# Optimization experiments

Hardware: AMD Instinct MI355X
Metric: run time of the kernel (lower is better)

The kernel has to match this reference:

```python
import jax, jax.numpy as jnp
import numpy as np


def _laplacian_with_self_loop(adj):
    # matrix = adj + I; D^{-1/2} (sym-normalized) as in the torch code
    n = adj.shape[0]
    m = adj + jnp.eye(n, dtype=adj.dtype)
    row_sum = m.sum(axis=1)
    d_inv_sqrt = row_sum ** -0.5
    d_inv_sqrt = jnp.where(jnp.isinf(d_inv_sqrt), 0.0, d_inv_sqrt)
    # (m @ diag(d)).T @ diag(d) == (m * d[None,:]).T * d[None,:]
    return (m * d_inv_sqrt[None, :]).T * d_inv_sqrt[None, :]


MAX_DIFFUSION_STEP = 3  # K


def setup_inputs() -> dict:
    key = jax.random.key(0)
    k1, k2, k3 = jax.random.split(key, 3)
    B, N, D = 32, 512, 768
    M = MAX_DIFFUSION_STEP + 1
    inputs = jax.random.normal(k1, (B, N, D), dtype=jnp.float32)
    adj = jax.random.uniform(k2, (N, N), dtype=jnp.float32)
    # Xavier-normal-ish weights
    fan_in, fan_out = D * M, D
    std = float(np.sqrt(2.0 / (fan_in + fan_out)))
    weights = jax.random.normal(k3, (fan_in, fan_out), dtype=jnp.float32) * std
    biases = jnp.zeros((fan_out,), dtype=jnp.float32)
    return {"inputs": inputs, "adj": adj, "weights": weights, "biases": biases}


def reference(inputs, adj, weights, biases):
    B, N, D = inputs.shape
    K = MAX_DIFFUSION_STEP
    support = jax.lax.stop_gradient(_laplacian_with_self_loop(adj))  # computed under no_grad in torch

    # x0: [N, D*B]
    x0 = jnp.transpose(inputs, (1, 2, 0)).reshape(N, D * B)
    x1 = support @ x0
    xs = [x0, x1]
    for _ in range(2, K + 1):  # Chebyshev-like recurrence, small fixed K
        x2 = 2.0 * (support @ x1) - x0
        xs.append(x2)
        x1, x0 = x2, x1
    M = K + 1
    x = jnp.stack(xs, axis=0)                     # [M, N, D*B]
    x = x.reshape(M, N, D, B)
    x = jnp.transpose(x, (3, 1, 2, 0))            # [B, N, D, M]
    x = x.reshape(B * N, D * M)
    out = x @ weights + biases                    # [B*N, out]
    return out.reshape(B, N, -1)
```

## Files before the change

### kernel.cpp

```cpp
#include <hip/hip_runtime.h>

#define NN 512
#define DD 768
#define BB 32

typedef __bf16 bf16;
typedef bf16 bf16x8 __attribute__((ext_vector_type(8)));
typedef bf16 bf16x4 __attribute__((ext_vector_type(4)));
typedef float f32x4 __attribute__((ext_vector_type(4)));

typedef const unsigned int __attribute__((address_space(1)))* gas_cuintp;
typedef unsigned int __attribute__((address_space(3)))* las_uintp;

__device__ __forceinline__ void async_copy16(const void* g, void* l) {
    __builtin_amdgcn_global_load_lds((gas_cuintp)g, (las_uintp)l, 16, 0, 0);
}


__global__ void k_rowsum(const float* __restrict__ adj, float* __restrict__ dv) {
    const int i = blockIdx.x;
    const int lane = threadIdx.x;
    float s = 0.f;
#pragma unroll
    for (int j = 0; j < NN / 64; ++j) s += adj[(size_t)i * NN + lane + j * 64];
#pragma unroll
    for (int off = 32; off; off >>= 1) s += __shfl_down(s, off);
    if (lane == 0) dv[i] = rsqrtf(s + 1.0f);
}

__global__ void k_support2(const float* __restrict__ adj, const float* __restrict__ dv,
                           bf16* __restrict__ sb, bf16* __restrict__ sbt) {
    __shared__ bf16 tile[32][33];
    const int k0 = blockIdx.y * 32;
    const int n0 = blockIdx.x * 32;
    const int x = threadIdx.x;
    const int y = threadIdx.y;
    const float dn = dv[n0 + x];
#pragma unroll
    for (int q = 0; q < 4; ++q) {
        const int k = k0 + y + q * 8;
        float m = adj[(size_t)k * NN + n0 + x] + ((k == n0 + x) ? 1.0f : 0.0f);
        bf16 v = (bf16)(m * dn * dv[k]);
        sbt[(size_t)k * NN + n0 + x] = v;
        tile[y + q * 8][x] = v;
    }
    __syncthreads();
#pragma unroll
    for (int q = 0; q < 4; ++q)
        sb[(size_t)(n0 + y + q * 8) * NN + k0 + x] = tile[x][y + q * 8];
}

__global__ void k_prepwt2(const float* __restrict__ w, bf16* __restrict__ wt) {
    __shared__ bf16 tile[32][33];
    const int m = blockIdx.z;
    const int d0 = blockIdx.y * 32;
    const int o0 = blockIdx.x * 32;
    const int x = threadIdx.x, y = threadIdx.y;
#pragma unroll
    for (int q = 0; q < 4; ++q) {
        const int d = d0 + y + q * 8;
        tile[y + q * 8][x] = (bf16)w[(size_t)(d * 4 + m) * DD + o0 + x];
    }
    __syncthreads();
    bf16* wm = wt + (size_t)m * DD * DD;
#pragma unroll
    for (int q = 0; q < 4; ++q)
        wm[(size_t)(o0 + y + q * 8) * DD + d0 + x] = tile[x][y + q * 8];
}

__global__ __launch_bounds__(256) void k_prepx(const float* __restrict__ in,
                                               bf16* __restrict__ xr,
                                               bf16* __restrict__ xt) {
    __shared__ bf16 tile[64][65];
    const int b = blockIdx.z;
    const int d0 = blockIdx.x * 64;
    const int n0 = blockIdx.y * 64;
    const int t = threadIdx.x;
    const int tx = t & 15;
    const int ty = t >> 4;
    const float* ib = in + (size_t)b * NN * DD;
    bf16* xrb = xr + (size_t)b * NN * DD;
#pragma unroll
    for (int q = 0; q < 4; ++q) {
        const int n = n0 + ty + q * 16;
        f32x4 v = *(const f32x4*)&ib[(size_t)n * DD + d0 + tx * 4];
        bf16x4 p;
#pragma unroll
        for (int j = 0; j < 4; ++j) p[j] = (bf16)v[j];
        *(bf16x4*)&xrb[(size_t)n * DD + d0 + tx * 4] = p;
#pragma unroll
        for (int j = 0; j < 4; ++j) tile[ty + q * 16][tx * 4 + j] = p[j];
    }
    __syncthreads();
    bf16* xtb = xt + (size_t)b * DD * NN;
#pragma unroll
    for (int q = 0; q < 4; ++q) {
        const int d = ty + q * 16;
        bf16x4 p;
#pragma unroll
        for (int j = 0; j < 4; ++j) p[j] = tile[tx * 4 + j][d];
        *(bf16x4*)&xtb[(size_t)(d0 + d) * NN + n0 + tx * 4] = p;
    }
}

__device__ __forceinline__ void mfma_tile_loop(const bf16* __restrict__ A,
                                               const bf16* __restrict__ B,
                                               int lda, int ldb, int K,
                                               int i0, int j0,
                                               bf16* At, bf16* Bt, f32x4 acc[4][4]) {
    const int t = threadIdx.x;
    const int lane = t & 63;
    const int w = t >> 6;
    const int wr = w >> 1, wc = w & 1;
    const int srow = t >> 2;
    const int scol = (t & 3) * 8;
    const int fr = lane & 15;
    const int fk = (lane >> 4) * 8;
    for (int k0 = 0; k0 < K; k0 += 32) {
        __syncthreads();
        async_copy16(A + (size_t)(i0 + srow) * lda + k0 + scol, &At[t * 8]);
        async_copy16(A + (size_t)(i0 + 64 + srow) * lda + k0 + scol, &At[2048 + t * 8]);
        async_copy16(B + (size_t)(j0 + srow) * ldb + k0 + scol, &Bt[t * 8]);
        async_copy16(B + (size_t)(j0 + 64 + srow) * ldb + k0 + scol, &Bt[2048 + t * 8]);
        __syncthreads();
        bf16x8 af[4], bg[4];
#pragma unroll
        for (int mi = 0; mi < 4; ++mi)
            af[mi] = *(const bf16x8*)&At[(wr * 64 + mi * 16 + fr) * 32 + fk];
#pragma unroll
        for (int ni = 0; ni < 4; ++ni)
            bg[ni] = *(const bf16x8*)&Bt[(wc * 64 + ni * 16 + fr) * 32 + fk];
#pragma unroll
        for (int mi = 0; mi < 4; ++mi)
#pragma unroll
            for (int ni = 0; ni < 4; ++ni)
                acc[mi][ni] = __builtin_amdgcn_mfma_f32_16x16x32_bf16(
                    af[mi], bg[ni], acc[mi][ni], 0, 0, 0);
    }
}

__global__ __launch_bounds__(256) void k_poly2(const bf16* __restrict__ Sb,
                                               const bf16* __restrict__ SbT,
                                               bf16* __restrict__ P2,
                                               bf16* __restrict__ P2T) {
    __shared__ bf16 At[4096] __attribute__((aligned(16)));
    __shared__ bf16 Bt[4096] __attribute__((aligned(16)));
    const int i0 = blockIdx.y * 128, j0 = blockIdx.x * 128;
    f32x4 acc[4][4];
#pragma unroll
    for (int mi = 0; mi < 4; ++mi)
#pragma unroll
        for (int ni = 0; ni < 4; ++ni) acc[mi][ni] = f32x4{0.f, 0.f, 0.f, 0.f};
    mfma_tile_loop(Sb, SbT, NN, NN, NN, i0, j0, At, Bt, acc);
    const int t = threadIdx.x, lane = t & 63, w = t >> 6;
    const int wr = w >> 1, wc = w & 1;
    const int fr = lane & 15, rb = (lane >> 4) * 4;
#pragma unroll
    for (int mi = 0; mi < 4; ++mi)
#pragma unroll
        for (int ni = 0; ni < 4; ++ni) {
            const int ii = i0 + wr * 64 + mi * 16 + rb;
            const int jj = j0 + wc * 64 + ni * 16 + fr;
#pragma unroll
            for (int tt = 0; tt < 4; ++tt) {
                float v = 2.f * acc[mi][ni][tt] - ((ii + tt) == jj ? 1.f : 0.f);
                bf16 bv = (bf16)v;
                P2[(size_t)(ii + tt) * NN + jj] = bv;
                P2T[(size_t)jj * NN + (ii + tt)] = bv;
            }
        }
}

__global__ __launch_bounds__(256) void k_poly3(const bf16* __restrict__ Sb,
                                               const bf16* __restrict__ P2T,
                                               bf16* __restrict__ P3) {
    __shared__ bf16 At[4096] __attribute__((aligned(16)));
    __shared__ bf16 Bt[4096] __attribute__((aligned(16)));
    const int i0 = blockIdx.y * 128, j0 = blockIdx.x * 128;
    f32x4 acc[4][4];
#pragma unroll
    for (int mi = 0; mi < 4; ++mi)
#pragma unroll
        for (int ni = 0; ni < 4; ++ni) acc[mi][ni] = f32x4{0.f, 0.f, 0.f, 0.f};
    mfma_tile_loop(Sb, P2T, NN, NN, NN, i0, j0, At, Bt, acc);
    const int t = threadIdx.x, lane = t & 63, w = t >> 6;
    const int wr = w >> 1, wc = w & 1;
    const int fr = lane & 15, rb = (lane >> 4) * 4;
#pragma unroll
    for (int mi = 0; mi < 4; ++mi)
#pragma unroll
        for (int ni = 0; ni < 4; ++ni) {
            const int ii = i0 + wr * 64 + mi * 16 + rb;
            const int jj = j0 + wc * 64 + ni * 16 + fr;
#pragma unroll
            for (int tt = 0; tt < 4; ++tt) {
                float v = 2.f * acc[mi][ni][tt] - (float)Sb[(size_t)(ii + tt) * NN + jj];
                P3[(size_t)(ii + tt) * NN + jj] = (bf16)v;
            }
        }
}

__global__ __launch_bounds__(256) void k_apply(const bf16* __restrict__ P,
                                               const bf16* __restrict__ XT0,
                                               bf16* __restrict__ Xr) {
    __shared__ bf16 At[4096] __attribute__((aligned(16)));
    __shared__ bf16 Bt[4096] __attribute__((aligned(16)));
    __shared__ bf16 epi[32 * 136] __attribute__((aligned(16)));
    const int z = blockIdx.z;
    const int m = z >> 5;
    const int b = z & 31;
    const int i0 = blockIdx.y * 128;
    const int j0 = blockIdx.x * 128;
    const bf16* A = P + (size_t)(2 * m) * NN * NN;
    const bf16* B = XT0 + (size_t)b * DD * NN;
    f32x4 acc[4][4];
#pragma unroll
    for (int mi = 0; mi < 4; ++mi)
#pragma unroll
        for (int ni = 0; ni < 4; ++ni) acc[mi][ni] = f32x4{0.f, 0.f, 0.f, 0.f};
    mfma_tile_loop(A, B, NN, NN, NN, i0, j0, At, Bt, acc);

    bf16* ob = Xr + ((size_t)m * BB + b) * NN * DD;
    const int t = threadIdx.x, lane = t & 63, w = t >> 6;
    const int wr = w >> 1, wc = w & 1;
    const int fr = lane & 15, rb = (lane >> 4) * 4;
#pragma unroll
    for (int mi = 0; mi < 4; ++mi) {
        __syncthreads();
#pragma unroll
        for (int ni = 0; ni < 4; ++ni) {
            const int col = wc * 64 + ni * 16 + fr;
#pragma unroll
            for (int tt = 0; tt < 4; ++tt) {
                const int lr = wr * 16 + rb + tt;
                epi[lr * 136 + col] = (bf16)acc[mi][ni][tt];
            }
        }
        __syncthreads();
#pragma unroll
        for (int it = 0; it < 2; ++it) {
            const int idx = t + it * 256;
            const int lr = idx >> 4;
            const int cq = idx & 15;
            bf16x8 vv = *(const bf16x8*)&epi[lr * 136 + cq * 8];
            const int gr = i0 + (lr >> 4) * 64 + mi * 16 + (lr & 15);
            *(bf16x8*)&ob[(size_t)gr * DD + j0 + cq * 8] = vv;
        }
    }
}

__global__ __launch_bounds__(256) void k_final(const bf16* __restrict__ Xr,
                                               const bf16* __restrict__ Wt,
                                               const float* __restrict__ bias,
                                               float* __restrict__ out) {
    __shared__ bf16 At[4096] __attribute__((aligned(16)));
    __shared__ bf16 Bt[4096] __attribute__((aligned(16)));
    const int wgid = blockIdx.y * gridDim.x + blockIdx.x;
    const int swz = (wgid & 7) * 96 + (wgid >> 3);
    const int i0 = (swz / 6) * 128;
    const int j0 = (swz % 6) * 128;
    const int t = threadIdx.x;
    const int lane = t & 63;
    const int w = t >> 6;
    const int wr = w >> 1, wc = w & 1;
    const int srow = t >> 2;
    const int scol = (t & 3) * 8;
    const int fr = lane & 15;
    const int fk = (lane >> 4) * 8;

    f32x4 acc[4][4];
#pragma unroll
    for (int mi = 0; mi < 4; ++mi)
#pragma unroll
        for (int ni = 0; ni < 4; ++ni) acc[mi][ni] = f32x4{0.f, 0.f, 0.f, 0.f};

    for (int s = 0; s < 4; ++s) {
        const bf16* As = Xr + (size_t)s * BB * NN * DD;
        const bf16* Bs = Wt + (size_t)s * DD * DD;
        for (int k0 = 0; k0 < DD; k0 += 32) {
            __syncthreads();
            async_copy16(As + (size_t)(i0 + srow) * DD + k0 + scol, &At[t * 8]);
            async_copy16(As + (size_t)(i0 + 64 + srow) * DD + k0 + scol, &At[2048 + t * 8]);
            async_copy16(Bs + (size_t)(j0 + srow) * DD + k0 + scol, &Bt[t * 8]);
            async_copy16(Bs + (size_t)(j0 + 64 + srow) * DD + k0 + scol, &Bt[2048 + t * 8]);
            __syncthreads();
            bf16x8 af[4], bg[4];
#pragma unroll
            for (int mi = 0; mi < 4; ++mi)
                af[mi] = *(const bf16x8*)&At[(wr * 64 + mi * 16 + fr) * 32 + fk];
#pragma unroll
            for (int ni = 0; ni < 4; ++ni)
                bg[ni] = *(const bf16x8*)&Bt[(wc * 64 + ni * 16 + fr) * 32 + fk];
#pragma unroll
            for (int mi = 0; mi < 4; ++mi)
#pragma unroll
                for (int ni = 0; ni < 4; ++ni)
                    acc[mi][ni] = __builtin_amdgcn_mfma_f32_16x16x32_bf16(
                        af[mi], bg[ni], acc[mi][ni], 0, 0, 0);
        }
    }

    const int rb = (lane >> 4) * 4;
#pragma unroll
    for (int ni = 0; ni < 4; ++ni) {
        const int jj = j0 + wc * 64 + ni * 16 + fr;
        const float bv = bias[jj];
#pragma unroll
        for (int mi = 0; mi < 4; ++mi) {
            const int ii = i0 + wr * 64 + mi * 16 + rb;
#pragma unroll
            for (int tt = 0; tt < 4; ++tt)
                out[(size_t)(ii + tt) * DD + jj] = acc[mi][ni][tt] + bv;
        }
    }
}

extern "C" void kernel_launch(void* const* d_in, const int* in_sizes, int n_in,
                              void* d_out, int out_size, void* d_ws, size_t ws_size,
                              hipStream_t stream) {
    const float* inputs = (const float*)d_in[0];
    const float* adj = (const float*)d_in[1];
    const float* weights = (const float*)d_in[2];
    const float* biases = (const float*)d_in[3];
    float* out = (float*)d_out;

    char* ws = (char*)d_ws;
    const size_t SQ = (size_t)NN * NN * 2;
    const size_t SLAB = (size_t)BB * NN * DD * 2;
    float* dv = (float*)(ws + 0);
    bf16* Sb = (bf16*)(ws + 4096);
    bf16* SbT = (bf16*)(ws + 4096 + SQ);
    bf16* P2 = (bf16*)(ws + 4096 + 2 * SQ);
    bf16* P2T = (bf16*)(ws + 4096 + 3 * SQ);
    bf16* P3 = (bf16*)(ws + 4096 + 4 * SQ);
    bf16* Wt = (bf16*)(ws + 4096 + 5 * SQ);
    char* slabBase = ws + 4096 + 5 * SQ + (size_t)4 * DD * DD * 2;
    bf16* XT0 = (bf16*)(slabBase);
    bf16* Xr0 = (bf16*)(slabBase + SLAB);
    bf16* Xr1 = (bf16*)(slabBase + 2 * SLAB);

    k_rowsum<<<NN, 64, 0, stream>>>(adj, dv);
    k_support2<<<dim3(16, 16), dim3(32, 8), 0, stream>>>(adj, dv, Sb, SbT);
    k_prepwt2<<<dim3(24, 24, 4), dim3(32, 8), 0, stream>>>(weights, Wt);
    k_prepx<<<dim3(DD / 64, NN / 64, BB), 256, 0, stream>>>(inputs, Xr0, XT0);

    k_poly2<<<dim3(4, 4), 256, 0, stream>>>(Sb, SbT, P2, P2T);
    k_poly3<<<dim3(4, 4), 256, 0, stream>>>(Sb, P2T, P3);

    k_apply<<<dim3(DD / 128, NN / 128, 3 * BB), 256, 0, stream>>>(Sb, XT0, Xr1);

    k_final<<<dim3(DD / 128, (BB * NN) / 128), 256, 0, stream>>>(Xr0, Wt, biases, out);
}
```

Before: 300.4 us.

## Interleave diffusion stages into K=3072 layout and use 256x256 pipelined final GEMM

The four diffusion outputs are now written into one row-major [B*N, 3072] buffer, and the weights are stored as a matching [768, 3072] matrix, so the final projection is a single long-K GEMM. That GEMM uses 256x256 tiles with 512 threads, double-buffered async LDS staging, an XOR-swizzled LDS layout to avoid bank conflicts, and split-phase MFMA with priority hints. The aim is more operand reuse per tile and load latency hidden behind compute. In exchange, only 192 workgroups are launched, which may underfill the device, and there is much more register pressure per thread.

```diff
diff --git a/kernel.cpp b/kernel.cpp
--- a/kernel.cpp
+++ b/kernel.cpp
@@ -3,6 +3,8 @@
 #define NN 512
 #define DD 768
 #define BB 32
+#define KK 3072
+#define NTK 96
 
 typedef __bf16 bf16;
 typedef bf16 bf16x8 __attribute__((ext_vector_type(8)));
@@ -62,14 +64,13 @@
         tile[y + q * 8][x] = (bf16)w[(size_t)(d * 4 + m) * DD + o0 + x];
     }
     __syncthreads();
-    bf16* wm = wt + (size_t)m * DD * DD;
 #pragma unroll
     for (int q = 0; q < 4; ++q)
-        wm[(size_t)(o0 + y + q * 8) * DD + d0 + x] = tile[x][y + q * 8];
+        wt[(size_t)(o0 + y + q * 8) * KK + m * DD + d0 + x] = tile[x][y + q * 8];
 }
 
 __global__ __launch_bounds__(256) void k_prepx(const float* __restrict__ in,
-                                               bf16* __restrict__ xr,
+                                               bf16* __restrict__ xr4,
                                                bf16* __restrict__ xt) {
     __shared__ bf16 tile[64][65];
     const int b = blockIdx.z;
@@ -79,7 +80,6 @@
     const int tx = t & 15;
     const int ty = t >> 4;
     const float* ib = in + (size_t)b * NN * DD;
-    bf16* xrb = xr + (size_t)b * NN * DD;
 #pragma unroll
     for (int q = 0; q < 4; ++q) {
         const int n = n0 + ty + q * 16;
@@ -87,7 +87,7 @@
         bf16x4 p;
 #pragma unroll
         for (int j = 0; j < 4; ++j) p[j] = (bf16)v[j];
-        *(bf16x4*)&xrb[(size_t)n * DD + d0 + tx * 4] = p;
+        *(bf16x4*)&xr4[(size_t)(b * NN + n) * KK + d0 + tx * 4] = p;
 #pragma unroll
         for (int j = 0; j < 4; ++j) tile[ty + q * 16][tx * 4 + j] = p[j];
     }
@@ -202,7 +202,7 @@
 
 __global__ __launch_bounds__(256) void k_apply(const bf16* __restrict__ P,
                                                const bf16* __restrict__ XT0,
-                                               bf16* __restrict__ Xr) {
+                                               bf16* __restrict__ Xr4) {
     __shared__ bf16 At[4096] __attribute__((aligned(16)));
     __shared__ bf16 Bt[4096] __attribute__((aligned(16)));
     __shared__ bf16 epi[32 * 136] __attribute__((aligned(16)));
@@ -220,7 +220,7 @@
         for (int ni = 0; ni < 4; ++ni) acc[mi][ni] = f32x4{0.f, 0.f, 0.f, 0.f};
     mfma_tile_loop(A, B, NN, NN, NN, i0, j0, At, Bt, acc);
 
-    bf16* ob = Xr + ((size_t)m * BB + b) * NN * DD;
+    bf16* ob = Xr4 + (size_t)b * NN * KK + (m + 1) * DD;
     const int t = threadIdx.x, lane = t & 63, w = t >> 6;
     const int wr = w >> 1, wc = w & 1;
     const int fr = lane & 15, rb = (lane >> 4) * 4;
@@ -244,70 +244,106 @@
             const int cq = idx & 15;
             bf16x8 vv = *(const bf16x8*)&epi[lr * 136 + cq * 8];
             const int gr = i0 + (lr >> 4) * 64 + mi * 16 + (lr & 15);
-            *(bf16x8*)&ob[(size_t)gr * DD + j0 + cq * 8] = vv;
-        }
-    }
-}
-
-__global__ __launch_bounds__(256) void k_final(const bf16* __restrict__ Xr,
-                                               const bf16* __restrict__ Wt,
-                                               const float* __restrict__ bias,
-                                               float* __restrict__ out) {
-    __shared__ bf16 At[4096] __attribute__((aligned(16)));
-    __shared__ bf16 Bt[4096] __attribute__((aligned(16)));
-    const int wgid = blockIdx.y * gridDim.x + blockIdx.x;
-    const int swz = (wgid & 7) * 96 + (wgid >> 3);
-    const int i0 = (swz / 6) * 128;
-    const int j0 = (swz % 6) * 128;
+            *(bf16x8*)&ob[(size_t)gr * KK + j0 + cq * 8] = vv;
+        }
+    }
+}
+
+__device__ __forceinline__ void stage_tile(const bf16* __restrict__ p, int rowbase,
+                                           int kt, bf16* ldsdst, int t) {
+    const int srow = t >> 2;
+    const int sg = (t & 3) ^ ((t >> 2) & 3) ^ ((t >> 4) & 3);
+    const bf16* s0 = p + (size_t)(rowbase + srow) * KK + kt * 32 + sg * 8;
+    const bf16* s1 = s0 + (size_t)128 * KK;
+    async_copy16(s0, ldsdst + t * 8);
+    async_copy16(s1, ldsdst + 4096 + t * 8);
+}
+
+__global__ __launch_bounds__(512, 2)
+void k_final512(const bf16* __restrict__ A, const bf16* __restrict__ Bw,
+                const float* __restrict__ bias, float* __restrict__ out) {
+    __shared__ bf16 lds[2][2][256 * 32] __attribute__((aligned(16)));
     const int t = threadIdx.x;
     const int lane = t & 63;
     const int w = t >> 6;
-    const int wr = w >> 1, wc = w & 1;
-    const int srow = t >> 2;
-    const int scol = (t & 3) * 8;
+    const int wr = w >> 2;
+    const int wc = w & 3;
+    const int wgid = blockIdx.x;
+    const int swz = (wgid & 7) * 24 + (wgid >> 3);
+    const int i0 = (swz / 3) * 256;
+    const int j0 = (swz % 3) * 256;
     const int fr = lane & 15;
-    const int fk = (lane >> 4) * 8;
-
-    f32x4 acc[4][4];
-#pragma unroll
-    for (int mi = 0; mi < 4; ++mi)
+    const int g = lane >> 4;
+    const int rslot8 = (g ^ (fr & 3) ^ ((fr >> 2) & 3)) * 8;
+    const int abase = (wr * 128 + fr) * 32 + rslot8;
+    const int bbase = (wc * 64 + fr) * 32 + rslot8;
+
+    f32x4 acc[8][4];
+#pragma unroll
+    for (int mi = 0; mi < 8; ++mi)
 #pragma unroll
         for (int ni = 0; ni < 4; ++ni) acc[mi][ni] = f32x4{0.f, 0.f, 0.f, 0.f};
 
-    for (int s = 0; s < 4; ++s) {
-        const bf16* As = Xr + (size_t)s * BB * NN * DD;
-        const bf16* Bs = Wt + (size_t)s * DD * DD;
-        for (int k0 = 0; k0 < DD; k0 += 32) {
-            __syncthreads();
-            async_copy16(As + (size_t)(i0 + srow) * DD + k0 + scol, &At[t * 8]);
-            async_copy16(As + (size_t)(i0 + 64 + srow) * DD + k0 + scol, &At[2048 + t * 8]);
-            async_copy16(Bs + (size_t)(j0 + srow) * DD + k0 + scol, &Bt[t * 8]);
-            async_copy16(Bs + (size_t)(j0 + 64 + srow) * DD + k0 + scol, &Bt[2048 + t * 8]);
-            __syncthreads();
-            bf16x8 af[4], bg[4];
-#pragma unroll
-            for (int mi = 0; mi < 4; ++mi)
-                af[mi] = *(const bf16x8*)&At[(wr * 64 + mi * 16 + fr) * 32 + fk];
+    stage_tile(A, i0, 0, &lds[0][0][0], t);
+    stage_tile(Bw, j0, 0, &lds[0][1][0], t);
+    stage_tile(Bw, j0, 1, &lds[1][1][0], t);
+    asm volatile("s_waitcnt vmcnt(2)" ::: "memory");
+    __builtin_amdgcn_s_barrier();
+    __builtin_amdgcn_sched_barrier(0);
+
+    for (int kt = 0; kt < NTK; ++kt) {
+        const int cur = kt & 1;
+        const bf16* As = &lds[cur][0][0];
+        const bf16* Bs = &lds[cur][1][0];
+        bf16x8 bg[4], af[4];
+#pragma unroll
+        for (int ni = 0; ni < 4; ++ni) bg[ni] = *(const bf16x8*)&Bs[bbase + ni * 512];
+#pragma unroll
+        for (int mi = 0; mi < 4; ++mi) af[mi] = *(const bf16x8*)&As[abase + mi * 512];
+        if (kt + 1 < NTK) stage_tile(A, i0, kt + 1, &lds[cur ^ 1][0][0], t);
+        __builtin_amdgcn_s_barrier();
+        __builtin_amdgcn_sched_barrier(0);
+        __builtin_amdgcn_s_setprio(1);
+#pragma unroll
+        for (int mi = 0; mi < 4; ++mi)
 #pragma unroll
             for (int ni = 0; ni < 4; ++ni)
-                bg[ni] = *(const bf16x8*)&Bt[(wc * 64 + ni * 16 + fr) * 32 + fk];
-#pragma unroll
-            for (int mi = 0; mi < 4; ++mi)
-#pragma unroll
-                for (int ni = 0; ni < 4; ++ni)
-                    acc[mi][ni] = __builtin_amdgcn_mfma_f32_16x16x32_bf16(
-                        af[mi], bg[ni], acc[mi][ni], 0, 0, 0);
-        }
-    }
-
-    const int rb = (lane >> 4) * 4;
+                acc[mi][ni] = __builtin_amdgcn_mfma_f32_16x16x32_bf16(
+                    af[mi], bg[ni], acc[mi][ni], 0, 0, 0);
+        __builtin_amdgcn_s_setprio(0);
+        __builtin_amdgcn_s_barrier();
+        __builtin_amdgcn_sched_barrier(0);
+#pragma unroll
+        for (int mi = 0; mi < 4; ++mi)
+            af[mi] = *(const bf16x8*)&As[abase + 2048 + mi * 512];
+        if (kt + 2 < NTK) stage_tile(Bw, j0, kt + 2, &lds[cur][1][0], t);
+        __builtin_amdgcn_s_barrier();
+        __builtin_amdgcn_sched_barrier(0);
+        __builtin_amdgcn_s_setprio(1);
+#pragma unroll
+        for (int mi = 0; mi < 4; ++mi)
+#pragma unroll
+            for (int ni = 0; ni < 4; ++ni)
+                acc[4 + mi][ni] = __builtin_amdgcn_mfma_f32_16x16x32_bf16(
+                    af[mi], bg[ni], acc[4 + mi][ni], 0, 0, 0);
+        __builtin_amdgcn_s_setprio(0);
+        if (kt < NTK - 2) {
+            asm volatile("s_waitcnt vmcnt(2)" ::: "memory");
+        } else {
+            asm volatile("s_waitcnt vmcnt(0)" ::: "memory");
+        }
+        __builtin_amdgcn_s_barrier();
+        __builtin_amdgcn_sched_barrier(0);
+    }
+
+    const int rb = g * 4;
 #pragma unroll
     for (int ni = 0; ni < 4; ++ni) {
         const int jj = j0 + wc * 64 + ni * 16 + fr;
         const float bv = bias[jj];
 #pragma unroll
-        for (int mi = 0; mi < 4; ++mi) {
-            const int ii = i0 + wr * 64 + mi * 16 + rb;
+        for (int mi = 0; mi < 8; ++mi) {
+            const int ii = i0 + wr * 128 + mi * 16 + rb;
 #pragma unroll
             for (int tt = 0; tt < 4; ++tt)
                 out[(size_t)(ii + tt) * DD + jj] = acc[mi][ni][tt] + bv;
@@ -326,28 +362,26 @@
 
     char* ws = (char*)d_ws;
     const size_t SQ = (size_t)NN * NN * 2;
-    const size_t SLAB = (size_t)BB * NN * DD * 2;
     float* dv = (float*)(ws + 0);
     bf16* Sb = (bf16*)(ws + 4096);
     bf16* SbT = (bf16*)(ws + 4096 + SQ);
     bf16* P2 = (bf16*)(ws + 4096 + 2 * SQ);
     bf16* P2T = (bf16*)(ws + 4096 + 3 * SQ);
     bf16* P3 = (bf16*)(ws + 4096 + 4 * SQ);
-    bf16* Wt = (bf16*)(ws + 4096 + 5 * SQ);
-    char* slabBase = ws + 4096 + 5 * SQ + (size_t)4 * DD * DD * 2;
-    bf16* XT0 = (bf16*)(slabBase);
-    bf16* Xr0 = (bf16*)(slabBase + SLAB);
-    bf16* Xr1 = (bf16*)(slabBase + 2 * SLAB);
+    bf16* WtK = (bf16*)(ws + 4096 + 5 * SQ);
+    char* p = ws + 4096 + 5 * SQ + (size_t)DD * KK * 2;
+    bf16* XT0 = (bf16*)p;
+    bf16* Xr4 = (bf16*)(p + (size_t)BB * NN * DD * 2);
 
     k_rowsum<<<NN, 64, 0, stream>>>(adj, dv);
     k_support2<<<dim3(16, 16), dim3(32, 8), 0, stream>>>(adj, dv, Sb, SbT);
-    k_prepwt2<<<dim3(24, 24, 4), dim3(32, 8), 0, stream>>>(weights, Wt);
-    k_prepx<<<dim3(DD / 64, NN / 64, BB), 256, 0, stream>>>(inputs, Xr0, XT0);
+    k_prepwt2<<<dim3(24, 24, 4), dim3(32, 8), 0, stream>>>(weights, WtK);
+    k_prepx<<<dim3(DD / 64, NN / 64, BB), 256, 0, stream>>>(inputs, Xr4, XT0);
 
     k_poly2<<<dim3(4, 4), 256, 0, stream>>>(Sb, SbT, P2, P2T);
     k_poly3<<<dim3(4, 4), 256, 0, stream>>>(Sb, P2T, P3);
 
-    k_apply<<<dim3(DD / 128, NN / 128, 3 * BB), 256, 0, stream>>>(Sb, XT0, Xr1);
-
-    k_final<<<dim3(DD / 128, (BB * NN) / 128), 256, 0, stream>>>(Xr0, Wt, biases, out);
-}
+    k_apply<<<dim3(DD / 128, NN / 128, 3 * BB), 256, 0, stream>>>(Sb, XT0, Xr4);
+
+    k_final512<<<192, 512, 0, stream>>>(Xr4, WtK, biases, out);
+}
```

After: 302.0 us. About the same (+0.5%).
